# Optimization experiments

Hardware: AMD Instinct MI355X
Metric: run time of the kernel (lower is better)

The kernel has to match this reference:

```python
import jax, jax.numpy as jnp
import numpy as np

B, S, H, E = 8, 2048, 1024, 8
CAP_FACTOR = 1.25  # deepspeed-style capacity factor for top-1 gating


def setup_inputs() -> dict:
    key = jax.random.key(0)
    ks = jax.random.split(key, 10)
    sc = 0.02
    return {
        "x": jax.random.normal(ks[0], (B, S, H), jnp.float32),
        "W_in": jax.random.normal(ks[1], (H, H), jnp.float32) * sc,
        "b_in": jnp.zeros((H,), jnp.float32),
        "W_gate": jax.random.normal(ks[2], (H, E), jnp.float32) * sc,
        "W1": jax.random.normal(ks[3], (E, H, H), jnp.float32) * sc,
        "b1": jnp.zeros((E, H), jnp.float32),
        "W2": jax.random.normal(ks[4], (E, H, H), jnp.float32) * sc,
        "b2": jnp.zeros((E, H), jnp.float32),
        "Wr1": jax.random.normal(ks[5], (H, H), jnp.float32) * sc,
        "br1": jnp.zeros((H,), jnp.float32),
        "Wr2": jax.random.normal(ks[6], (H, H), jnp.float32) * sc,
        "br2": jnp.zeros((H,), jnp.float32),
        "W_coef": jax.random.normal(ks[7], (H, 2), jnp.float32) * sc,
        "b_coef": jnp.zeros((2,), jnp.float32),
        "W_out": jax.random.normal(ks[8], (H, H), jnp.float32) * sc,
        "b_out": jnp.zeros((H,), jnp.float32),
    }


def _moe(x, W_gate, W1, b1, W2, b2, Wr1, br1, Wr2, br2, W_coef, b_coef):
    # x: [T, H] flattened tokens. Top-1 gating with capacity dropping + residual expert.
    T, Hd = x.shape
    nE = W_gate.shape[1]
    cap = int(np.ceil(CAP_FACTOR * T / nE))  # static under jit

    gates = jax.nn.softmax(x @ W_gate)                  # [T, E]
    eidx = jnp.argmax(gates, axis=-1)                    # [T]
    mask1 = jax.nn.one_hot(eidx, nE, dtype=x.dtype)      # [T, E]
    pos = jnp.cumsum(mask1, axis=0) - 1.0                # position within each expert
    pos_tok = jnp.take_along_axis(pos, eidx[:, None], 1)[:, 0].astype(jnp.int32)
    keep = (pos_tok < cap).astype(x.dtype)               # capacity drop mask
    gate_val = jnp.take_along_axis(gates, eidx[:, None], 1)[:, 0] * keep  # [T]
    slot = jnp.minimum(pos_tok, cap - 1)                 # safe slot index

    # scatter tokens into [E, cap, H] buffers (dropped tokens contribute zeros)
    disp = jnp.zeros((nE, cap, Hd), x.dtype).at[eidx, slot].add(x * keep[:, None])
    h = jax.nn.relu(jnp.einsum('ech,ehf->ecf', disp, W1) + b1[:, None, :])
    eo = jnp.einsum('ecf,efg->ecg', h, W2) + b2[:, None, :]
    moe_out = eo[eidx, slot] * gate_val[:, None]         # gather back; dropped -> 0

    # residual expert on all tokens, mixed with learned 2-way softmax coefficient
    res = jax.nn.relu(x @ Wr1 + br1) @ Wr2 + br2
    coef = jax.nn.softmax(x @ W_coef + b_coef)           # [T, 2]
    return moe_out * coef[:, :1] + res * coef[:, 1:]


def reference(x, W_in, b_in, W_gate, W1, b1, W2, b2, Wr1, br1, Wr2, br2,
              W_coef, b_coef, W_out, b_out):
    Bb, Ss, Hd = x.shape
    t = x.reshape(-1, Hd) @ W_in + b_in
    t = _moe(t, W_gate, W1, b1, W2, b2, Wr1, br1, Wr2, br2, W_coef, b_coef)
    t = t @ W_out + b_out
    return t.reshape(Bb, Ss, Hd)
```

## Files before the change

### kernel.cpp

```cpp
#include <hip/hip_runtime.h>
#include <cstdint>

#define T_TOK 16384
#define HD    1024
#define NE    8
#define CAP   2560
#define NCHUNK (T_TOK / 64)

typedef __attribute__((ext_vector_type(4))) float f32x4;
typedef __attribute__((ext_vector_type(8))) short bf16x8;

__device__ __forceinline__ unsigned short f2bf(float f) {
    union { float f; unsigned u; } x{f};
    unsigned r = x.u + 0x7FFF + ((x.u >> 16) & 1);
    return (unsigned short)(r >> 16);
}

__device__ __forceinline__ void gload_lds16(const unsigned short* g, unsigned short* l) {
    __builtin_amdgcn_global_load_lds(
        (const __attribute__((address_space(1))) void*)g,
        (__attribute__((address_space(3))) void*)l, 16, 0, 0);
}

template<bool GATHER, bool RELU, bool ROWSCALE, bool SCATTER, bool OUTBF16>
__global__ __launch_bounds__(512)
void gemm_bf16_k(const unsigned short* __restrict__ A,
                 const unsigned short* __restrict__ Bt,
                 const float* __restrict__ bias,
                 void* __restrict__ Cv,
                 int M, int N, int K,
                 const int* __restrict__ idxTab,
                 const float* __restrict__ rs,
                 long aB, long bB, long biasB, long tabB, long cB)
{
    const int nx = gridDim.x, ny = gridDim.y;
    long nwg = (long)nx * ny * gridDim.z;
    long flat = blockIdx.x + (long)nx * (blockIdx.y + (long)ny * blockIdx.z);
    long cpx = nwg >> 3;
    long swz = (flat & 7) * cpx + (flat >> 3);
    const int bx = (int)(swz % nx);
    const int by = (int)((swz / nx) % ny);
    const int bz = (int)(swz / ((long)nx * ny));

    A  += (long)bz * aB;
    Bt += (long)bz * bB;
    const float* bptr = bias + (long)bz * biasB;
    const int* tab = idxTab ? idxTab + (long)bz * tabB : nullptr;
    float*          Cf = (float*)Cv + (long)bz * cB;
    unsigned short* Cb = (unsigned short*)Cv + (long)bz * cB;

    __shared__ unsigned short As[256][64];
    __shared__ unsigned short Bs[128][64];

    const int tid  = threadIdx.x;
    const int wv   = tid >> 6;
    const int lane = tid & 63;
    const int m0 = by * 256, n0 = bx * 128;

    const int srow = lane >> 3;
    const int schk = lane & 7;

    const unsigned short* aSrc[4];
    const unsigned short* bSrc[2];
    #pragma unroll
    for (int i = 0; i < 4; ++i) {
        int lrow = wv * 32 + i * 8 + srow;
        int scol = ((schk ^ (lrow & 7)) * 8);
        long sr;
        if (GATHER) { int tr = tab[m0 + lrow]; sr = tr < 0 ? 0 : tr; }
        else        sr = m0 + lrow;
        aSrc[i] = A + sr * (long)K + scol;
    }
    #pragma unroll
    for (int i = 0; i < 2; ++i) {
        int lrow = wv * 16 + i * 8 + srow;
        int scol = ((schk ^ (lrow & 7)) * 8);
        bSrc[i] = Bt + (long)(n0 + lrow) * K + scol;
    }

    f32x4 acc[4][4] = {};
    const int wm = wv >> 1, wn = wv & 1;
    const int fr = lane & 15, kg = lane >> 4;

    for (int k0 = 0; k0 < K; k0 += 64) {
        __syncthreads();
        #pragma unroll
        for (int i = 0; i < 4; ++i)
            gload_lds16(aSrc[i] + k0, &As[wv * 32 + i * 8][0]);
        #pragma unroll
        for (int i = 0; i < 2; ++i)
            gload_lds16(bSrc[i] + k0, &Bs[wv * 16 + i * 8][0]);
        __syncthreads();

        #pragma unroll
        for (int kk = 0; kk < 2; ++kk) {
            bf16x8 af[4], bfr[4];
            #pragma unroll
            for (int i2 = 0; i2 < 4; ++i2) {
                int R = wm * 64 + i2 * 16 + fr;
                af[i2] = *(const bf16x8*)&As[R][((kk * 4 + kg) ^ (R & 7)) * 8];
            }
            #pragma unroll
            for (int j2 = 0; j2 < 4; ++j2) {
                int R = wn * 64 + j2 * 16 + fr;
                bfr[j2] = *(const bf16x8*)&Bs[R][((kk * 4 + kg) ^ (R & 7)) * 8];
            }
            #pragma unroll
            for (int i2 = 0; i2 < 4; ++i2)
                #pragma unroll
                for (int j2 = 0; j2 < 4; ++j2)
                    acc[i2][j2] = __builtin_amdgcn_mfma_f32_16x16x32_bf16(
                        af[i2], bfr[j2], acc[i2][j2], 0, 0, 0);
        }
    }

    const int colL = lane & 15, rgrp = (lane >> 4) * 4;
    #pragma unroll
    for (int i2 = 0; i2 < 4; ++i2) {
        #pragma unroll
        for (int r = 0; r < 4; ++r) {
            int gm = m0 + wm * 64 + i2 * 16 + rgrp + r;
            int token = gm; float sc = 1.0f;
            if (SCATTER) {
                token = tab[gm];
                if (token < 0) continue;
                sc = rs[token];
            } else if (ROWSCALE) {
                sc = rs[gm];
            }
            #pragma unroll
            for (int j2 = 0; j2 < 4; ++j2) {
                int gn = n0 + wn * 64 + j2 * 16 + colL;
                float v = acc[i2][j2][r] + bptr[gn];
                if (RELU) v = fmaxf(v, 0.0f);
                if (SCATTER) {
                    Cf[(long)token * N + gn] += v * sc;
                } else {
                    if (ROWSCALE) v *= sc;
                    if (OUTBF16) Cb[(long)gm * N + gn] = f2bf(v);
                    else         Cf[(long)gm * N + gn] = v;
                }
            }
        }
    }
}

__global__ __launch_bounds__(256)
void cast_bf16_k(const float* __restrict__ in, unsigned short* __restrict__ out,
                 long n4)
{
    long i = (long)blockIdx.x * 256 + threadIdx.x;
    long stride = (long)gridDim.x * 256;
    for (; i < n4; i += stride) {
        float4 v = ((const float4*)in)[i];
        ushort4 o;
        o.x = f2bf(v.x); o.y = f2bf(v.y); o.z = f2bf(v.z); o.w = f2bf(v.w);
        ((ushort4*)out)[i] = o;
    }
}

__global__ __launch_bounds__(256)
void transpose_cast_k(const float* __restrict__ W, unsigned short* __restrict__ Wt,
                      int K, int N, long wB, long wtB)
{
    const int z = blockIdx.z;
    W  += (long)z * wB;
    Wt += (long)z * wtB;
    __shared__ float tile[64][65];
    const int k0 = blockIdx.x * 64, n0 = blockIdx.y * 64;
    const int c = threadIdx.x & 63, r4 = threadIdx.x >> 6;
    #pragma unroll 4
    for (int it = 0; it < 16; ++it) {
        int row = it * 4 + r4;
        tile[row][c] = W[(long)(k0 + row) * N + n0 + c];
    }
    __syncthreads();
    #pragma unroll 4
    for (int it = 0; it < 16; ++it) {
        int nrow = it * 4 + r4;
        Wt[(long)(n0 + nrow) * K + k0 + c] = f2bf(tile[c][nrow]);
    }
}

__global__ __launch_bounds__(256)
void wsmall_k(const float* __restrict__ W_in, const float* __restrict__ W_gate,
              const float* __restrict__ W_coef,
              float* __restrict__ wgp, float* __restrict__ wcp)
{
    const int r = blockIdx.x * 4 + (threadIdx.x >> 6);
    const int lane = threadIdx.x & 63;
    float s[10] = {};
    for (int k = lane; k < HD; k += 64) {
        float a = W_in[(long)r * HD + k];
        const float4* g = (const float4*)(W_gate + (long)k * 8);
        float4 g0 = g[0], g1 = g[1];
        s[0] += a * g0.x; s[1] += a * g0.y; s[2] += a * g0.z; s[3] += a * g0.w;
        s[4] += a * g1.x; s[5] += a * g1.y; s[6] += a * g1.z; s[7] += a * g1.w;
        float2 cv = *(const float2*)(W_coef + (long)k * 2);
        s[8] += a * cv.x; s[9] += a * cv.y;
    }
    #pragma unroll
    for (int off = 32; off > 0; off >>= 1)
        #pragma unroll
        for (int e = 0; e < 10; ++e) s[e] += __shfl_xor(s[e], off);
    if (lane == 0) {
        #pragma unroll
        for (int e = 0; e < 8; ++e) wgp[(long)r * 8 + e] = s[e];
        wcp[(long)r * 2 + 0] = s[8];
        wcp[(long)r * 2 + 1] = s[9];
    }
}

__global__ void gbias_k(const float* __restrict__ b_in, const float* __restrict__ W_gate,
                        const float* __restrict__ W_coef, const float* __restrict__ b_coef,
                        float* __restrict__ bg, float* __restrict__ bc)
{
    const int lane = threadIdx.x;
    float s[10] = {};
    for (int k = lane; k < HD; k += 64) {
        float a = b_in[k];
        const float4* g = (const float4*)(W_gate + (long)k * 8);
        float4 g0 = g[0], g1 = g[1];
        s[0] += a * g0.x; s[1] += a * g0.y; s[2] += a * g0.z; s[3] += a * g0.w;
        s[4] += a * g1.x; s[5] += a * g1.y; s[6] += a * g1.z; s[7] += a * g1.w;
        float2 cv = *(const float2*)(W_coef + (long)k * 2);
        s[8] += a * cv.x; s[9] += a * cv.y;
    }
    #pragma unroll
    for (int off = 32; off > 0; off >>= 1)
        #pragma unroll
        for (int e = 0; e < 10; ++e) s[e] += __shfl_xor(s[e], off);
    if (lane == 0) {
        #pragma unroll
        for (int e = 0; e < 8; ++e) bg[e] = s[e];
        bc[0] = s[8] + b_coef[0];
        bc[1] = s[9] + b_coef[1];
    }
}

__global__ __launch_bounds__(256)
void gating_k(const float* __restrict__ x,
              const float* __restrict__ Wg,
              const float* __restrict__ Wc,
              const float* __restrict__ bg,
              const float* __restrict__ bc,
              int* __restrict__ eidx,
              float* __restrict__ gval,
              float* __restrict__ coef0,
              float* __restrict__ coef1)
{
    const int tok = (blockIdx.x * 256 + threadIdx.x) >> 6;
    const int lane = threadIdx.x & 63;
    const float* row = x + (long)tok * HD;

    float acc[8] = {};
    float c0 = 0.f, c1 = 0.f;
    for (int i = 0; i < HD / 64; ++i) {
        int k = i * 64 + lane;
        float tv = row[k];
        const float4* wg = (const float4*)(Wg + (long)k * 8);
        float4 w0 = wg[0], w1 = wg[1];
        acc[0] = fmaf(tv, w0.x, acc[0]); acc[1] = fmaf(tv, w0.y, acc[1]);
        acc[2] = fmaf(tv, w0.z, acc[2]); acc[3] = fmaf(tv, w0.w, acc[3]);
        acc[4] = fmaf(tv, w1.x, acc[4]); acc[5] = fmaf(tv, w1.y, acc[5]);
        acc[6] = fmaf(tv, w1.z, acc[6]); acc[7] = fmaf(tv, w1.w, acc[7]);
        float2 wcv = *(const float2*)(Wc + (long)k * 2);
        c0 = fmaf(tv, wcv.x, c0);
        c1 = fmaf(tv, wcv.y, c1);
    }
    #pragma unroll
    for (int off = 32; off > 0; off >>= 1) {
        #pragma unroll
        for (int e = 0; e < 8; ++e) acc[e] += __shfl_xor(acc[e], off);
        c0 += __shfl_xor(c0, off);
        c1 += __shfl_xor(c1, off);
    }
    if (lane == 0) {
        #pragma unroll
        for (int e = 0; e < 8; ++e) acc[e] += bg[e];
        float m = acc[0]; int best = 0;
        #pragma unroll
        for (int e = 1; e < 8; ++e) if (acc[e] > m) { m = acc[e]; best = e; }
        float s = 0.f;
        #pragma unroll
        for (int e = 0; e < 8; ++e) s += expf(acc[e] - m);
        eidx[tok] = best;
        gval[tok] = 1.0f / s;
        float l0 = c0 + bc[0], l1 = c1 + bc[1];
        float mm = fmaxf(l0, l1);
        float e0 = expf(l0 - mm), e1 = expf(l1 - mm);
        float inv = 1.0f / (e0 + e1);
        coef0[tok] = e0 * inv;
        coef1[tok] = e1 * inv;
    }
}

__global__ void scan_hist_k(const int* __restrict__ eidx,
                            int* __restrict__ counts,
                            int* __restrict__ idxTab)
{
    const int b = blockIdx.x;
    const int lane = threadIdx.x;
    for (int j = b * 64 + lane; j < NE * CAP; j += NCHUNK * 64)
        idxTab[j] = -1;
    int e = eidx[b * 64 + lane];
    #pragma unroll
    for (int ex = 0; ex < NE; ++ex) {
        unsigned long long msk = __ballot(e == ex);
        if (lane == ex) counts[b * NE + ex] = (int)__popcll(msk);
    }
}

__global__ void scan_offsets_k(const int* __restrict__ counts,
                               int* __restrict__ offsets)
{
    const int e = threadIdx.x;
    if (e < NE) {
        int run = 0;
        for (int b = 0; b < NCHUNK; ++b) {
            offsets[b * NE + e] = run;
            run += counts[b * NE + e];
        }
    }
}

__global__ void scan_fill_k(const int* __restrict__ eidx,
                            const float* __restrict__ gval,
                            const float* __restrict__ coef0,
                            const int* __restrict__ offsets,
                            int* __restrict__ idxTab,
                            float* __restrict__ smoe)
{
    const int b = blockIdx.x;
    const int lane = threadIdx.x;
    const int tok = b * 64 + lane;
    int e = eidx[tok];
    unsigned long long below = (lane == 0) ? 0ull : ((~0ull) >> (64 - lane));
    int myrank = 0;
    #pragma unroll
    for (int ex = 0; ex < NE; ++ex) {
        unsigned long long msk = __ballot(e == ex);
        if (e == ex) myrank = (int)__popcll(msk & below) + offsets[b * NE + ex];
    }
    if (myrank < CAP) {
        idxTab[e * CAP + myrank] = tok;
        smoe[tok] = gval[tok] * coef0[tok];
    } else {
        smoe[tok] = 0.0f;
    }
}

extern "C" void kernel_launch(void* const* d_in, const int* in_sizes, int n_in,
                              void* d_out, int out_size, void* d_ws, size_t ws_size,
                              hipStream_t stream)
{
    const float* x      = (const float*)d_in[0];
    const float* W_in   = (const float*)d_in[1];
    const float* b_in   = (const float*)d_in[2];
    const float* W_gate = (const float*)d_in[3];
    const float* W1     = (const float*)d_in[4];
    const float* b1     = (const float*)d_in[5];
    const float* W2     = (const float*)d_in[6];
    const float* b2     = (const float*)d_in[7];
    const float* Wr1    = (const float*)d_in[8];
    const float* br1    = (const float*)d_in[9];
    const float* Wr2    = (const float*)d_in[10];
    const float* br2    = (const float*)d_in[11];
    const float* W_coef = (const float*)d_in[12];
    const float* b_coef = (const float*)d_in[13];
    const float* W_out  = (const float*)d_in[14];
    const float* b_out  = (const float*)d_in[15];
    float* out = (float*)d_out;

    const size_t MiB = 1024 * 1024;
    char* ws = (char*)d_ws;
    unsigned short* W1T  = (unsigned short*)(ws + 0);
    unsigned short* res1 = (unsigned short*)(ws + 0);
    unsigned short* mixb = (unsigned short*)(ws + 0);
    unsigned short* h    = (unsigned short*)(ws + 32 * MiB);
    unsigned short* t_b  = (unsigned short*)(ws + 72 * MiB);
    unsigned short* W2T  = (unsigned short*)(ws + 104 * MiB);
    unsigned short* WinT = (unsigned short*)(ws + 120 * MiB);
    unsigned short* Wr1T = (unsigned short*)(ws + 122 * MiB);
    unsigned short* Wr2T = (unsigned short*)(ws + 124 * MiB);
    unsigned short* WoutT= (unsigned short*)(ws + 126 * MiB);
    char* sm = ws + 128 * MiB;
    float* wgp  = (float*)(sm);            sm += HD * 8 * 4;
    float* wcp  = (float*)(sm);            sm += HD * 2 * 4;
    float* bg   = (float*)(sm);            sm += 64;
    float* bc   = (float*)(sm);            sm += 64;
    int*   eidx = (int*)(sm);              sm += T_TOK * 4;
    float* gval = (float*)(sm);            sm += T_TOK * 4;
    float* cf0  = (float*)(sm);            sm += T_TOK * 4;
    float* cf1  = (float*)(sm);            sm += T_TOK * 4;
    float* smoe = (float*)(sm);            sm += T_TOK * 4;
    int* idxTab = (int*)(sm);              sm += NE * CAP * 4;
    int* counts = (int*)(sm);              sm += NCHUNK * NE * 4;
    int* offs   = (int*)(sm);              sm += NCHUNK * NE * 4;
    unsigned short* xb = (unsigned short*)d_out;
    float* mix = out;
    (void)ws_size; (void)in_sizes; (void)n_in; (void)out_size;

    dim3 blk(256);
    dim3 blkG(512);
    dim3 gT(16, 16, 1);
    dim3 gT8(16, 16, 8);
    dim3 gBig(HD / 128, T_TOK / 256, 1);
    dim3 gExp(HD / 128, CAP / 256, NE);

    cast_bf16_k<<<2048, blk, 0, stream>>>(x, xb, (long)T_TOK * HD / 4);
    transpose_cast_k<<<gT,  blk, 0, stream>>>(W_in,  WinT,  HD, HD, 0, 0);
    transpose_cast_k<<<gT,  blk, 0, stream>>>(Wr1,   Wr1T,  HD, HD, 0, 0);
    transpose_cast_k<<<gT,  blk, 0, stream>>>(Wr2,   Wr2T,  HD, HD, 0, 0);
    transpose_cast_k<<<gT,  blk, 0, stream>>>(W_out, WoutT, HD, HD, 0, 0);
    transpose_cast_k<<<gT8, blk, 0, stream>>>(W1, W1T, HD, HD, (long)HD * HD, (long)HD * HD);
    transpose_cast_k<<<gT8, blk, 0, stream>>>(W2, W2T, HD, HD, (long)HD * HD, (long)HD * HD);
    wsmall_k<<<HD / 4, blk, 0, stream>>>(W_in, W_gate, W_coef, wgp, wcp);
    gbias_k<<<1, 64, 0, stream>>>(b_in, W_gate, W_coef, b_coef, bg, bc);
    gating_k<<<T_TOK / 4, blk, 0, stream>>>(x, wgp, wcp, bg, bc, eidx, gval, cf0, cf1);
    scan_hist_k<<<NCHUNK, 64, 0, stream>>>(eidx, counts, idxTab);
    scan_offsets_k<<<1, 64, 0, stream>>>(counts, offs);
    scan_fill_k<<<NCHUNK, 64, 0, stream>>>(eidx, gval, cf0, offs, idxTab, smoe);
    gemm_bf16_k<false, false, false, false, true><<<gBig, blkG, 0, stream>>>(
        xb, WinT, b_in, t_b, T_TOK, HD, HD, nullptr, nullptr, 0, 0, 0, 0, 0);
    gemm_bf16_k<true, true, false, false, true><<<gExp, blkG, 0, stream>>>(
        t_b, W1T, b1, h, CAP, HD, HD, idxTab, nullptr,
        0, (long)HD * HD, HD, CAP, (long)CAP * HD);
    gemm_bf16_k<false, true, false, false, true><<<gBig, blkG, 0, stream>>>(
        t_b, Wr1T, br1, res1, T_TOK, HD, HD, nullptr, nullptr, 0, 0, 0, 0, 0);
    gemm_bf16_k<false, false, true, false, false><<<gBig, blkG, 0, stream>>>(
        res1, Wr2T, br2, mix, T_TOK, HD, HD, nullptr, cf1, 0, 0, 0, 0, 0);
    gemm_bf16_k<false, false, false, true, false><<<gExp, blkG, 0, stream>>>(
        h, W2T, b2, mix, CAP, HD, HD, idxTab, smoe,
        (long)CAP * HD, (long)HD * HD, HD, CAP, 0);
    cast_bf16_k<<<2048, blk, 0, stream>>>(mix, mixb, (long)T_TOK * HD / 4);
    gemm_bf16_k<false, false, false, false, false><<<gBig, blkG, 0, stream>>>(
        mixb, WoutT, b_out, out, T_TOK, HD, HD, nullptr, nullptr, 0, 0, 0, 0, 0);
}
```

Measured before the change: 418.8 us.

## Fuse bf16 casts into gating and expert scatter epilogue, cast only dropped tokens

The input-to-bf16 cast is folded into the gating kernel, which already streams every row of x. The full fp32-to-bf16 pass over the mixed activations is removed. The second expert GEMM now writes bf16 directly, combining the residual fp32 value with the scaled expert output. A compacted list of capacity-dropped tokens, built with an atomic counter during the scan, drives a small kernel that casts only those rows. This eliminates two full-tensor memory passes, at the cost of an extra read in the scatter epilogue and narrower stores in gating.

```diff
diff --git a/kernel.cpp b/kernel.cpp
--- a/kernel.cpp
+++ b/kernel.cpp
@@ -31,6 +31,7 @@
                  int M, int N, int K,
                  const int* __restrict__ idxTab,
                  const float* __restrict__ rs,
+                 const float* __restrict__ addsrc,
                  long aB, long bB, long biasB, long tabB, long cB)
 {
     const int nx = gridDim.x, ny = gridDim.y;
@@ -134,7 +135,9 @@
                 float v = acc[i2][j2][r] + bptr[gn];
                 if (RELU) v = fmaxf(v, 0.0f);
                 if (SCATTER) {
-                    Cf[(long)token * N + gn] += v * sc;
+                    long idx = (long)token * N + gn;
+                    if (OUTBF16) Cb[idx] = f2bf(addsrc[idx] + v * sc);
+                    else         Cf[idx] += v * sc;
                 } else {
                     if (ROWSCALE) v *= sc;
                     if (OUTBF16) Cb[(long)gm * N + gn] = f2bf(v);
@@ -146,16 +149,19 @@
 }
 
 __global__ __launch_bounds__(256)
-void cast_bf16_k(const float* __restrict__ in, unsigned short* __restrict__ out,
-                 long n4)
-{
-    long i = (long)blockIdx.x * 256 + threadIdx.x;
-    long stride = (long)gridDim.x * 256;
-    for (; i < n4; i += stride) {
-        float4 v = ((const float4*)in)[i];
+void drop_cast_k(const float* __restrict__ mix, unsigned short* __restrict__ mixb,
+                 const int* __restrict__ droplist, const int* __restrict__ dropcnt)
+{
+    const int cnt = *dropcnt;
+    for (int i = blockIdx.x; i < cnt; i += gridDim.x) {
+        const int tok = droplist[i];
+        const float4* src = (const float4*)(mix + (long)tok * HD);
+        ushort4* dst = (ushort4*)(mixb + (long)tok * HD);
+        const int j = threadIdx.x;
+        float4 v = src[j];
         ushort4 o;
         o.x = f2bf(v.x); o.y = f2bf(v.y); o.z = f2bf(v.z); o.w = f2bf(v.w);
-        ((ushort4*)out)[i] = o;
+        dst[j] = o;
     }
 }
 
@@ -244,6 +250,7 @@
               const float* __restrict__ Wc,
               const float* __restrict__ bg,
               const float* __restrict__ bc,
+              unsigned short* __restrict__ xb,
               int* __restrict__ eidx,
               float* __restrict__ gval,
               float* __restrict__ coef0,
@@ -252,12 +259,14 @@
     const int tok = (blockIdx.x * 256 + threadIdx.x) >> 6;
     const int lane = threadIdx.x & 63;
     const float* row = x + (long)tok * HD;
+    unsigned short* orow = xb + (long)tok * HD;
 
     float acc[8] = {};
     float c0 = 0.f, c1 = 0.f;
     for (int i = 0; i < HD / 64; ++i) {
         int k = i * 64 + lane;
         float tv = row[k];
+        orow[k] = f2bf(tv);
         const float4* wg = (const float4*)(Wg + (long)k * 8);
         float4 w0 = wg[0], w1 = wg[1];
         acc[0] = fmaf(tv, w0.x, acc[0]); acc[1] = fmaf(tv, w0.y, acc[1]);
@@ -312,9 +321,11 @@
 }
 
 __global__ void scan_offsets_k(const int* __restrict__ counts,
-                               int* __restrict__ offsets)
+                               int* __restrict__ offsets,
+                               int* __restrict__ dropcnt)
 {
     const int e = threadIdx.x;
+    if (e == 63) *dropcnt = 0;
     if (e < NE) {
         int run = 0;
         for (int b = 0; b < NCHUNK; ++b) {
@@ -329,7 +340,9 @@
                             const float* __restrict__ coef0,
                             const int* __restrict__ offsets,
                             int* __restrict__ idxTab,
-                            float* __restrict__ smoe)
+                            float* __restrict__ smoe,
+                            int* __restrict__ droplist,
+                            int* __restrict__ dropcnt)
 {
     const int b = blockIdx.x;
     const int lane = threadIdx.x;
@@ -347,6 +360,8 @@
         smoe[tok] = gval[tok] * coef0[tok];
     } else {
         smoe[tok] = 0.0f;
+        int di = atomicAdd(dropcnt, 1);
+        droplist[di] = tok;
     }
 }
 
@@ -397,6 +412,8 @@
     int* idxTab = (int*)(sm);              sm += NE * CAP * 4;
     int* counts = (int*)(sm);              sm += NCHUNK * NE * 4;
     int* offs   = (int*)(sm);              sm += NCHUNK * NE * 4;
+    int* droplist = (int*)(sm);            sm += T_TOK * 4;
+    int* dropcnt  = (int*)(sm);            sm += 64;
     unsigned short* xb = (unsigned short*)d_out;
     float* mix = out;
     (void)ws_size; (void)in_sizes; (void)n_in; (void)out_size;
@@ -408,7 +425,6 @@
     dim3 gBig(HD / 128, T_TOK / 256, 1);
     dim3 gExp(HD / 128, CAP / 256, NE);
 
-    cast_bf16_k<<<2048, blk, 0, stream>>>(x, xb, (long)T_TOK * HD / 4);
     transpose_cast_k<<<gT,  blk, 0, stream>>>(W_in,  WinT,  HD, HD, 0, 0);
     transpose_cast_k<<<gT,  blk, 0, stream>>>(Wr1,   Wr1T,  HD, HD, 0, 0);
     transpose_cast_k<<<gT,  blk, 0, stream>>>(Wr2,   Wr2T,  HD, HD, 0, 0);
@@ -417,23 +433,29 @@
     transpose_cast_k<<<gT8, blk, 0, stream>>>(W2, W2T, HD, HD, (long)HD * HD, (long)HD * HD);
     wsmall_k<<<HD / 4, blk, 0, stream>>>(W_in, W_gate, W_coef, wgp, wcp);
     gbias_k<<<1, 64, 0, stream>>>(b_in, W_gate, W_coef, b_coef, bg, bc);
-    gating_k<<<T_TOK / 4, blk, 0, stream>>>(x, wgp, wcp, bg, bc, eidx, gval, cf0, cf1);
+    gating_k<<<T_TOK / 4, blk, 0, stream>>>(x, wgp, wcp, bg, bc, xb,
+                                            eidx, gval, cf0, cf1);
     scan_hist_k<<<NCHUNK, 64, 0, stream>>>(eidx, counts, idxTab);
-    scan_offsets_k<<<1, 64, 0, stream>>>(counts, offs);
-    scan_fill_k<<<NCHUNK, 64, 0, stream>>>(eidx, gval, cf0, offs, idxTab, smoe);
+    scan_offsets_k<<<1, 64, 0, stream>>>(counts, offs, dropcnt);
+    scan_fill_k<<<NCHUNK, 64, 0, stream>>>(eidx, gval, cf0, offs, idxTab, smoe,
+                                           droplist, dropcnt);
     gemm_bf16_k<false, false, false, false, true><<<gBig, blkG, 0, stream>>>(
-        xb, WinT, b_in, t_b, T_TOK, HD, HD, nullptr, nullptr, 0, 0, 0, 0, 0);
+        xb, WinT, b_in, t_b, T_TOK, HD, HD, nullptr, nullptr, nullptr,
+        0, 0, 0, 0, 0);
     gemm_bf16_k<true, true, false, false, true><<<gExp, blkG, 0, stream>>>(
-        t_b, W1T, b1, h, CAP, HD, HD, idxTab, nullptr,
+        t_b, W1T, b1, h, CAP, HD, HD, idxTab, nullptr, nullptr,
         0, (long)HD * HD, HD, CAP, (long)CAP * HD);
     gemm_bf16_k<false, true, false, false, true><<<gBig, blkG, 0, stream>>>(
-        t_b, Wr1T, br1, res1, T_TOK, HD, HD, nullptr, nullptr, 0, 0, 0, 0, 0);
+        t_b, Wr1T, br1, res1, T_TOK, HD, HD, nullptr, nullptr, nullptr,
+        0, 0, 0, 0, 0);
     gemm_bf16_k<false, false, true, false, false><<<gBig, blkG, 0, stream>>>(
-        res1, Wr2T, br2, mix, T_TOK, HD, HD, nullptr, cf1, 0, 0, 0, 0, 0);
-    gemm_bf16_k<false, false, false, true, false><<<gExp, blkG, 0, stream>>>(
-        h, W2T, b2, mix, CAP, HD, HD, idxTab, smoe,
+        res1, Wr2T, br2, mix, T_TOK, HD, HD, nullptr, cf1, nullptr,
+        0, 0, 0, 0, 0);
+    gemm_bf16_k<false, false, false, true, true><<<gExp, blkG, 0, stream>>>(
+        h, W2T, b2, mixb, CAP, HD, HD, idxTab, smoe, mix,
         (long)CAP * HD, (long)HD * HD, HD, CAP, 0);
-    cast_bf16_k<<<2048, blk, 0, stream>>>(mix, mixb, (long)T_TOK * HD / 4);
+    drop_cast_k<<<256, blk, 0, stream>>>(mix, mixb, droplist, dropcnt);
     gemm_bf16_k<false, false, false, false, false><<<gBig, blkG, 0, stream>>>(
-        mixb, WoutT, b_out, out, T_TOK, HD, HD, nullptr, nullptr, 0, 0, 0, 0, 0);
-}
+        mixb, WoutT, b_out, out, T_TOK, HD, HD, nullptr, nullptr, nullptr,
+        0, 0, 0, 0, 0);
+}
```

Result: faster. 405.3 us (-3.2%).

## Fold W_in and W_out into expert and residual weights to drop token GEMMs

Applied to the files above, without the earlier changes.

The linear input and output projections are folded algebraically into the expert and residual weights. Small bf16 weight-by-weight GEMMs build W_in·W1, W_in·Wr1, Wr2·W_out and W2·W_out, and vector-matrix kernels build the matching folded biases. This removes the two full token-sized GEMMs, the intermediate t buffer and the final mix cast. It also fuses the x-to-bf16 cast into the gating kernel and adds an early exit for empty expert tiles. In exchange it adds a batched weight-fusion GEMM and extra bf16 rounding of the product weights, which may change numerics slightly.

```diff
diff --git a/kernel.cpp b/kernel.cpp
--- a/kernel.cpp
+++ b/kernel.cpp
@@ -31,6 +31,7 @@
                  int M, int N, int K,
                  const int* __restrict__ idxTab,
                  const float* __restrict__ rs,
+                 const float* __restrict__ post,
                  long aB, long bB, long biasB, long tabB, long cB)
 {
     const int nx = gridDim.x, ny = gridDim.y;
@@ -44,18 +45,21 @@
 
     A  += (long)bz * aB;
     Bt += (long)bz * bB;
-    const float* bptr = bias + (long)bz * biasB;
+    const float* bptr = bias ? bias + (long)bz * biasB : nullptr;
     const int* tab = idxTab ? idxTab + (long)bz * tabB : nullptr;
     float*          Cf = (float*)Cv + (long)bz * cB;
     unsigned short* Cb = (unsigned short*)Cv + (long)bz * cB;
 
+    const int m0 = by * 256, n0 = bx * 128;
+
+    if ((GATHER || SCATTER) && tab[m0] < 0) return;
+
     __shared__ unsigned short As[256][64];
     __shared__ unsigned short Bs[128][64];
 
     const int tid  = threadIdx.x;
     const int wv   = tid >> 6;
     const int lane = tid & 63;
-    const int m0 = by * 256, n0 = bx * 128;
 
     const int srow = lane >> 3;
     const int schk = lane & 7;
@@ -131,12 +135,14 @@
             #pragma unroll
             for (int j2 = 0; j2 < 4; ++j2) {
                 int gn = n0 + wn * 64 + j2 * 16 + colL;
-                float v = acc[i2][j2][r] + bptr[gn];
+                float v = acc[i2][j2][r] + (bptr ? bptr[gn] : 0.0f);
                 if (RELU) v = fmaxf(v, 0.0f);
                 if (SCATTER) {
                     Cf[(long)token * N + gn] += v * sc;
                 } else {
-                    if (ROWSCALE) v *= sc;
+                    if (ROWSCALE) {
+                        v = v * sc + (post ? post[gn] : 0.0f);
+                    }
                     if (OUTBF16) Cb[(long)gm * N + gn] = f2bf(v);
                     else         Cf[(long)gm * N + gn] = v;
                 }
@@ -180,6 +186,30 @@
         int nrow = it * 4 + r4;
         Wt[(long)(n0 + nrow) * K + k0 + c] = f2bf(tile[c][nrow]);
     }
+}
+
+__global__ void vecmat_init_k(const float* __restrict__ badd, long bB,
+                              float* __restrict__ out, long oB)
+{
+    const int z = blockIdx.y;
+    const int n = blockIdx.x * 256 + threadIdx.x;
+    out[z * oB + n] = badd ? badd[z * bB + n] : 0.0f;
+}
+
+__global__ void vecmat_acc_k(const float* __restrict__ v, long vB,
+                             const float* __restrict__ W, long wB,
+                             float* __restrict__ out, long oB)
+{
+    const int z = blockIdx.z;
+    const int n = blockIdx.x * 256 + threadIdx.x;
+    const int kc = blockIdx.y;
+    const float* vp = v + z * vB;
+    const float* Wp = W + z * wB;
+    float acc = 0.f;
+    #pragma unroll 8
+    for (int k = kc * 128; k < kc * 128 + 128; ++k)
+        acc = fmaf(vp[k], Wp[(long)k * HD + n], acc);
+    atomicAdd(out + z * oB + n, acc);
 }
 
 __global__ __launch_bounds__(256)
@@ -244,6 +274,7 @@
               const float* __restrict__ Wc,
               const float* __restrict__ bg,
               const float* __restrict__ bc,
+              unsigned short* __restrict__ xb,
               int* __restrict__ eidx,
               float* __restrict__ gval,
               float* __restrict__ coef0,
@@ -252,12 +283,14 @@
     const int tok = (blockIdx.x * 256 + threadIdx.x) >> 6;
     const int lane = threadIdx.x & 63;
     const float* row = x + (long)tok * HD;
+    unsigned short* orow = xb + (long)tok * HD;
 
     float acc[8] = {};
     float c0 = 0.f, c1 = 0.f;
     for (int i = 0; i < HD / 64; ++i) {
         int k = i * 64 + lane;
         float tv = row[k];
+        orow[k] = f2bf(tv);
         const float4* wg = (const float4*)(Wg + (long)k * 8);
         float4 w0 = wg[0], w1 = wg[1];
         acc[0] = fmaf(tv, w0.x, acc[0]); acc[1] = fmaf(tv, w0.y, acc[1]);
@@ -374,21 +407,27 @@
 
     const size_t MiB = 1024 * 1024;
     char* ws = (char*)d_ws;
-    unsigned short* W1T  = (unsigned short*)(ws + 0);
-    unsigned short* res1 = (unsigned short*)(ws + 0);
-    unsigned short* mixb = (unsigned short*)(ws + 0);
-    unsigned short* h    = (unsigned short*)(ws + 32 * MiB);
-    unsigned short* t_b  = (unsigned short*)(ws + 72 * MiB);
-    unsigned short* W2T  = (unsigned short*)(ws + 104 * MiB);
-    unsigned short* WinT = (unsigned short*)(ws + 120 * MiB);
-    unsigned short* Wr1T = (unsigned short*)(ws + 122 * MiB);
-    unsigned short* Wr2T = (unsigned short*)(ws + 124 * MiB);
-    unsigned short* WoutT= (unsigned short*)(ws + 126 * MiB);
-    char* sm = ws + 128 * MiB;
+    unsigned short* W1T   = (unsigned short*)(ws + 0);
+    unsigned short* Wr1T  = (unsigned short*)(ws + 16 * MiB);
+    unsigned short* Winp  = (unsigned short*)(ws + 18 * MiB);
+    unsigned short* Wr2p  = (unsigned short*)(ws + 20 * MiB);
+    unsigned short* W2p   = (unsigned short*)(ws + 22 * MiB);
+    unsigned short* WoutT = (unsigned short*)(ws + 38 * MiB);
+    unsigned short* h     = (unsigned short*)(ws + 0);
+    unsigned short* WF1T  = (unsigned short*)(ws + 40 * MiB);
+    unsigned short* WFr1T = (unsigned short*)(ws + 56 * MiB);
+    unsigned short* WFr2T = (unsigned short*)(ws + 58 * MiB);
+    unsigned short* WF2T  = (unsigned short*)(ws + 60 * MiB);
+    unsigned short* res1  = (unsigned short*)(ws + 76 * MiB);
+    char* sm = ws + 108 * MiB;
     float* wgp  = (float*)(sm);            sm += HD * 8 * 4;
     float* wcp  = (float*)(sm);            sm += HD * 2 * 4;
     float* bg   = (float*)(sm);            sm += 64;
     float* bc   = (float*)(sm);            sm += 64;
+    float* bf1  = (float*)(sm);            sm += NE * HD * 4;
+    float* bfr1 = (float*)(sm);            sm += HD * 4;
+    float* c2   = (float*)(sm);            sm += HD * 4;
+    float* c3   = (float*)(sm);            sm += NE * HD * 4;
     int*   eidx = (int*)(sm);              sm += T_TOK * 4;
     float* gval = (float*)(sm);            sm += T_TOK * 4;
     float* cf0  = (float*)(sm);            sm += T_TOK * 4;
@@ -398,42 +437,56 @@
     int* counts = (int*)(sm);              sm += NCHUNK * NE * 4;
     int* offs   = (int*)(sm);              sm += NCHUNK * NE * 4;
     unsigned short* xb = (unsigned short*)d_out;
-    float* mix = out;
     (void)ws_size; (void)in_sizes; (void)n_in; (void)out_size;
 
+    const long HD2 = (long)HD * HD;
     dim3 blk(256);
     dim3 blkG(512);
     dim3 gT(16, 16, 1);
     dim3 gT8(16, 16, 8);
     dim3 gBig(HD / 128, T_TOK / 256, 1);
     dim3 gExp(HD / 128, CAP / 256, NE);
-
-    cast_bf16_k<<<2048, blk, 0, stream>>>(x, xb, (long)T_TOK * HD / 4);
-    transpose_cast_k<<<gT,  blk, 0, stream>>>(W_in,  WinT,  HD, HD, 0, 0);
+    dim3 gFuse(HD / 128, HD / 256, 9);
+
+    transpose_cast_k<<<gT8, blk, 0, stream>>>(W1, W1T, HD, HD, HD2, HD2);
     transpose_cast_k<<<gT,  blk, 0, stream>>>(Wr1,   Wr1T,  HD, HD, 0, 0);
-    transpose_cast_k<<<gT,  blk, 0, stream>>>(Wr2,   Wr2T,  HD, HD, 0, 0);
     transpose_cast_k<<<gT,  blk, 0, stream>>>(W_out, WoutT, HD, HD, 0, 0);
-    transpose_cast_k<<<gT8, blk, 0, stream>>>(W1, W1T, HD, HD, (long)HD * HD, (long)HD * HD);
-    transpose_cast_k<<<gT8, blk, 0, stream>>>(W2, W2T, HD, HD, (long)HD * HD, (long)HD * HD);
+    cast_bf16_k<<<512,  blk, 0, stream>>>(W_in, Winp, HD2 / 4);
+    cast_bf16_k<<<512,  blk, 0, stream>>>(Wr2,  Wr2p, HD2 / 4);
+    cast_bf16_k<<<2048, blk, 0, stream>>>(W2,   W2p,  (long)NE * HD2 / 4);
     wsmall_k<<<HD / 4, blk, 0, stream>>>(W_in, W_gate, W_coef, wgp, wcp);
     gbias_k<<<1, 64, 0, stream>>>(b_in, W_gate, W_coef, b_coef, bg, bc);
-    gating_k<<<T_TOK / 4, blk, 0, stream>>>(x, wgp, wcp, bg, bc, eidx, gval, cf0, cf1);
+    { dim3 gi(HD / 256, NE), ga(HD / 256, NE, NE);
+      vecmat_init_k<<<dim3(HD/256, NE), blk, 0, stream>>>(b1, HD, bf1, HD);
+      vecmat_acc_k <<<dim3(HD/256, 8, NE), blk, 0, stream>>>(b_in, 0, W1, HD2, bf1, HD);
+      vecmat_init_k<<<dim3(HD/256, 1), blk, 0, stream>>>(br1, 0, bfr1, 0);
+      vecmat_acc_k <<<dim3(HD/256, 8, 1), blk, 0, stream>>>(b_in, 0, Wr1, 0, bfr1, 0);
+      vecmat_init_k<<<dim3(HD/256, 1), blk, 0, stream>>>(nullptr, 0, c2, 0);
+      vecmat_acc_k <<<dim3(HD/256, 8, 1), blk, 0, stream>>>(br2, 0, W_out, 0, c2, 0);
+      vecmat_init_k<<<dim3(HD/256, NE), blk, 0, stream>>>(nullptr, 0, c3, HD);
+      vecmat_acc_k <<<dim3(HD/256, 8, NE), blk, 0, stream>>>(b2, HD, W_out, 0, c3, HD);
+    }
+    gating_k<<<T_TOK / 4, blk, 0, stream>>>(x, wgp, wcp, bg, bc, xb,
+                                            eidx, gval, cf0, cf1);
     scan_hist_k<<<NCHUNK, 64, 0, stream>>>(eidx, counts, idxTab);
     scan_offsets_k<<<1, 64, 0, stream>>>(counts, offs);
     scan_fill_k<<<NCHUNK, 64, 0, stream>>>(eidx, gval, cf0, offs, idxTab, smoe);
-    gemm_bf16_k<false, false, false, false, true><<<gBig, blkG, 0, stream>>>(
-        xb, WinT, b_in, t_b, T_TOK, HD, HD, nullptr, nullptr, 0, 0, 0, 0, 0);
+    gemm_bf16_k<false, false, false, false, true><<<gFuse, blkG, 0, stream>>>(
+        W1T, Winp, nullptr, WF1T, HD, HD, HD, nullptr, nullptr, nullptr,
+        HD2, 0, 0, 0, HD2);
+    gemm_bf16_k<false, false, false, false, true><<<gFuse, blkG, 0, stream>>>(
+        WoutT, Wr2p, nullptr, WFr2T, HD, HD, HD, nullptr, nullptr, nullptr,
+        0, HD2, 0, 0, HD2);
     gemm_bf16_k<true, true, false, false, true><<<gExp, blkG, 0, stream>>>(
-        t_b, W1T, b1, h, CAP, HD, HD, idxTab, nullptr,
-        0, (long)HD * HD, HD, CAP, (long)CAP * HD);
+        xb, WF1T, bf1, h, CAP, HD, HD, idxTab, nullptr, nullptr,
+        0, HD2, HD, CAP, (long)CAP * HD);
     gemm_bf16_k<false, true, false, false, true><<<gBig, blkG, 0, stream>>>(
-        t_b, Wr1T, br1, res1, T_TOK, HD, HD, nullptr, nullptr, 0, 0, 0, 0, 0);
+        xb, WFr1T, bfr1, res1, T_TOK, HD, HD, nullptr, nullptr, nullptr,
+        0, 0, 0, 0, 0);
     gemm_bf16_k<false, false, true, false, false><<<gBig, blkG, 0, stream>>>(
-        res1, Wr2T, br2, mix, T_TOK, HD, HD, nullptr, cf1, 0, 0, 0, 0, 0);
+        res1, WFr2T, c2, out, T_TOK, HD, HD, nullptr, cf1, b_out,
+        0, 0, 0, 0, 0);
     gemm_bf16_k<false, false, false, true, false><<<gExp, blkG, 0, stream>>>(
-        h, W2T, b2, mix, CAP, HD, HD, idxTab, smoe,
-        (long)CAP * HD, (long)HD * HD, HD, CAP, 0);
-    cast_bf16_k<<<2048, blk, 0, stream>>>(mix, mixb, (long)T_TOK * HD / 4);
-    gemm_bf16_k<false, false, false, false, false><<<gBig, blkG, 0, stream>>>(
-        mixb, WoutT, b_out, out, T_TOK, HD, HD, nullptr, nullptr, 0, 0, 0, 0, 0);
-}
+        h, WF2T, c3, out, CAP, HD, HD, idxTab, smoe, nullptr,
+        (long)CAP * HD, HD2, HD, CAP, 0);
+}
```

After: 459.9 us. 9.8% more time.

## Fuse bf16 casts into gating and GEMM epilogues, skip empty expert tiles

Applied to the files above, without the earlier changes.

The input cast to bf16 moves into the gating kernel, which already reads x. The residual and expert-scatter GEMMs now write the mix buffer directly in bf16, so the separate fp32 mix buffer and its cast kernel go away, and the scatter does a bf16 read-modify-write. GEMM blocks whose first gathered row is empty (unused capacity) now exit early. These changes remove two full elementwise passes and some wasted expert-tile work. The cost is an extra bf16 rounding when the residual and expert outputs are added together.

```diff
diff --git a/kernel.cpp b/kernel.cpp
--- a/kernel.cpp
+++ b/kernel.cpp
@@ -14,6 +14,12 @@
     union { float f; unsigned u; } x{f};
     unsigned r = x.u + 0x7FFF + ((x.u >> 16) & 1);
     return (unsigned short)(r >> 16);
+}
+
+__device__ __forceinline__ float bf2f(unsigned short b) {
+    union { unsigned u; float f; } x;
+    x.u = ((unsigned)b) << 16;
+    return x.f;
 }
 
 __device__ __forceinline__ void gload_lds16(const unsigned short* g, unsigned short* l) {
@@ -44,18 +50,21 @@
 
     A  += (long)bz * aB;
     Bt += (long)bz * bB;
-    const float* bptr = bias + (long)bz * biasB;
+    const float* bptr = bias ? bias + (long)bz * biasB : nullptr;
     const int* tab = idxTab ? idxTab + (long)bz * tabB : nullptr;
     float*          Cf = (float*)Cv + (long)bz * cB;
     unsigned short* Cb = (unsigned short*)Cv + (long)bz * cB;
 
+    const int m0 = by * 256, n0 = bx * 128;
+
+    if ((GATHER || SCATTER) && tab[m0] < 0) return;
+
     __shared__ unsigned short As[256][64];
     __shared__ unsigned short Bs[128][64];
 
     const int tid  = threadIdx.x;
     const int wv   = tid >> 6;
     const int lane = tid & 63;
-    const int m0 = by * 256, n0 = bx * 128;
 
     const int srow = lane >> 3;
     const int schk = lane & 7;
@@ -131,10 +140,15 @@
             #pragma unroll
             for (int j2 = 0; j2 < 4; ++j2) {
                 int gn = n0 + wn * 64 + j2 * 16 + colL;
-                float v = acc[i2][j2][r] + bptr[gn];
+                float v = acc[i2][j2][r] + (bptr ? bptr[gn] : 0.0f);
                 if (RELU) v = fmaxf(v, 0.0f);
                 if (SCATTER) {
-                    Cf[(long)token * N + gn] += v * sc;
+                    long idx = (long)token * N + gn;
+                    if (OUTBF16) {
+                        Cb[idx] = f2bf(bf2f(Cb[idx]) + v * sc);
+                    } else {
+                        Cf[idx] += v * sc;
+                    }
                 } else {
                     if (ROWSCALE) v *= sc;
                     if (OUTBF16) Cb[(long)gm * N + gn] = f2bf(v);
@@ -142,20 +156,6 @@
                 }
             }
         }
-    }
-}
-
-__global__ __launch_bounds__(256)
-void cast_bf16_k(const float* __restrict__ in, unsigned short* __restrict__ out,
-                 long n4)
-{
-    long i = (long)blockIdx.x * 256 + threadIdx.x;
-    long stride = (long)gridDim.x * 256;
-    for (; i < n4; i += stride) {
-        float4 v = ((const float4*)in)[i];
-        ushort4 o;
-        o.x = f2bf(v.x); o.y = f2bf(v.y); o.z = f2bf(v.z); o.w = f2bf(v.w);
-        ((ushort4*)out)[i] = o;
     }
 }
 
@@ -244,6 +244,7 @@
               const float* __restrict__ Wc,
               const float* __restrict__ bg,
               const float* __restrict__ bc,
+              unsigned short* __restrict__ xb,
               int* __restrict__ eidx,
               float* __restrict__ gval,
               float* __restrict__ coef0,
@@ -252,12 +253,14 @@
     const int tok = (blockIdx.x * 256 + threadIdx.x) >> 6;
     const int lane = threadIdx.x & 63;
     const float* row = x + (long)tok * HD;
+    unsigned short* orow = xb + (long)tok * HD;
 
     float acc[8] = {};
     float c0 = 0.f, c1 = 0.f;
     for (int i = 0; i < HD / 64; ++i) {
         int k = i * 64 + lane;
         float tv = row[k];
+        orow[k] = f2bf(tv);
         const float4* wg = (const float4*)(Wg + (long)k * 8);
         float4 w0 = wg[0], w1 = wg[1];
         acc[0] = fmaf(tv, w0.x, acc[0]); acc[1] = fmaf(tv, w0.y, acc[1]);
@@ -376,9 +379,9 @@
     char* ws = (char*)d_ws;
     unsigned short* W1T  = (unsigned short*)(ws + 0);
     unsigned short* res1 = (unsigned short*)(ws + 0);
-    unsigned short* mixb = (unsigned short*)(ws + 0);
     unsigned short* h    = (unsigned short*)(ws + 32 * MiB);
     unsigned short* t_b  = (unsigned short*)(ws + 72 * MiB);
+    unsigned short* mixb = (unsigned short*)(ws + 72 * MiB);
     unsigned short* W2T  = (unsigned short*)(ws + 104 * MiB);
     unsigned short* WinT = (unsigned short*)(ws + 120 * MiB);
     unsigned short* Wr1T = (unsigned short*)(ws + 122 * MiB);
@@ -398,7 +401,6 @@
     int* counts = (int*)(sm);              sm += NCHUNK * NE * 4;
     int* offs   = (int*)(sm);              sm += NCHUNK * NE * 4;
     unsigned short* xb = (unsigned short*)d_out;
-    float* mix = out;
     (void)ws_size; (void)in_sizes; (void)n_in; (void)out_size;
 
     dim3 blk(256);
@@ -408,7 +410,6 @@
     dim3 gBig(HD / 128, T_TOK / 256, 1);
     dim3 gExp(HD / 128, CAP / 256, NE);
 
-    cast_bf16_k<<<2048, blk, 0, stream>>>(x, xb, (long)T_TOK * HD / 4);
     transpose_cast_k<<<gT,  blk, 0, stream>>>(W_in,  WinT,  HD, HD, 0, 0);
     transpose_cast_k<<<gT,  blk, 0, stream>>>(Wr1,   Wr1T,  HD, HD, 0, 0);
     transpose_cast_k<<<gT,  blk, 0, stream>>>(Wr2,   Wr2T,  HD, HD, 0, 0);
@@ -417,23 +418,27 @@
     transpose_cast_k<<<gT8, blk, 0, stream>>>(W2, W2T, HD, HD, (long)HD * HD, (long)HD * HD);
     wsmall_k<<<HD / 4, blk, 0, stream>>>(W_in, W_gate, W_coef, wgp, wcp);
     gbias_k<<<1, 64, 0, stream>>>(b_in, W_gate, W_coef, b_coef, bg, bc);
-    gating_k<<<T_TOK / 4, blk, 0, stream>>>(x, wgp, wcp, bg, bc, eidx, gval, cf0, cf1);
+    gating_k<<<T_TOK / 4, blk, 0, stream>>>(x, wgp, wcp, bg, bc, xb,
+                                            eidx, gval, cf0, cf1);
     scan_hist_k<<<NCHUNK, 64, 0, stream>>>(eidx, counts, idxTab);
     scan_offsets_k<<<1, 64, 0, stream>>>(counts, offs);
     scan_fill_k<<<NCHUNK, 64, 0, stream>>>(eidx, gval, cf0, offs, idxTab, smoe);
     gemm_bf16_k<false, false, false, false, true><<<gBig, blkG, 0, stream>>>(
-        xb, WinT, b_in, t_b, T_TOK, HD, HD, nullptr, nullptr, 0, 0, 0, 0, 0);
+        xb, WinT, b_in, t_b, T_TOK, HD, HD, nullptr, nullptr,
+        0, 0, 0, 0, 0);
     gemm_bf16_k<true, true, false, false, true><<<gExp, blkG, 0, stream>>>(
         t_b, W1T, b1, h, CAP, HD, HD, idxTab, nullptr,
         0, (long)HD * HD, HD, CAP, (long)CAP * HD);
     gemm_bf16_k<false, true, false, false, true><<<gBig, blkG, 0, stream>>>(
-        t_b, Wr1T, br1, res1, T_TOK, HD, HD, nullptr, nullptr, 0, 0, 0, 0, 0);
-    gemm_bf16_k<false, false, true, false, false><<<gBig, blkG, 0, stream>>>(
-        res1, Wr2T, br2, mix, T_TOK, HD, HD, nullptr, cf1, 0, 0, 0, 0, 0);
-    gemm_bf16_k<false, false, false, true, false><<<gExp, blkG, 0, stream>>>(
-        h, W2T, b2, mix, CAP, HD, HD, idxTab, smoe,
+        t_b, Wr1T, br1, res1, T_TOK, HD, HD, nullptr, nullptr,
+        0, 0, 0, 0, 0);
+    gemm_bf16_k<false, false, true, false, true><<<gBig, blkG, 0, stream>>>(
+        res1, Wr2T, br2, mixb, T_TOK, HD, HD, nullptr, cf1,
+        0, 0, 0, 0, 0);
+    gemm_bf16_k<false, false, false, true, true><<<gExp, blkG, 0, stream>>>(
+        h, W2T, b2, mixb, CAP, HD, HD, idxTab, smoe,
         (long)CAP * HD, (long)HD * HD, HD, CAP, 0);
-    cast_bf16_k<<<2048, blk, 0, stream>>>(mix, mixb, (long)T_TOK * HD / 4);
     gemm_bf16_k<false, false, false, false, false><<<gBig, blkG, 0, stream>>>(
-        mixb, WoutT, b_out, out, T_TOK, HD, HD, nullptr, nullptr, 0, 0, 0, 0, 0);
-}
+        mixb, WoutT, b_out, out, T_TOK, HD, HD, nullptr, nullptr,
+        0, 0, 0, 0, 0);
+}
```

After: 443.2 us. 1.06x slower.
